# Performance work log

Hardware: AMD Instinct MI355X
Metric: run time of the kernel (lower is better)

## Reference

```python
import jax, jax.numpy as jnp
import numpy as np

D = 128          # embed_features
N = 4096         # cells per batch
M = 8192         # genes / regions
FB1, FB2, FR, FA = 100, 100, 256, 512


def setup_inputs() -> dict:
    key = jax.random.key(0)
    ks = jax.random.split(key, 16)
    s = 0.05  # weight scale to keep activations in a sane range
    return {
        "u1": jax.random.normal(ks[0], (N, FB1), jnp.float32),
        "u2": jax.random.normal(ks[1], (N, FB2), jnp.float32),
        "v1": jax.random.normal(ks[2], (M, FR), jnp.float32),
        "v2": jax.random.normal(ks[3], (M, FA), jnp.float32),
        # linear layers stored as [in, out] so y = x @ W
        "Wb1": jax.random.normal(ks[4], (FB1, D), jnp.float32) * s,
        "Wb2": jax.random.normal(ks[5], (FB2, D), jnp.float32) * s,
        "Wrna1": jax.random.normal(ks[6], (FR, 2 * D), jnp.float32) * s,
        "Wrna2": jax.random.normal(ks[7], (2 * D, D), jnp.float32) * s,
        "gene_act": jax.random.normal(ks[8], (FA, FR), jnp.float32) * s,
        "w_prod1": jax.random.normal(ks[9], (D,), jnp.float32),
        "w_add1": jax.random.normal(ks[10], (2 * D,), jnp.float32),
        "w_prod2": jax.random.normal(ks[11], (D,), jnp.float32),
        "w_add2": jax.random.normal(ks[12], (2 * D,), jnp.float32),
        "bias_1": jax.random.normal(ks[13], (), jnp.float32),
        "bias_2": jax.random.normal(ks[14], (), jnp.float32),
    }


def _pair_scores(eu, ev, w_prod, w_add, bias):
    # Algebraically identical to the original all-pairs form:
    #   (eu[:,None,:] * ev[None,:,:]) @ w_prod  ==  (eu * w_prod) @ ev.T
    #   cat(eu, ev) @ w_add  ==  eu @ w_add[:D]  +  ev @ w_add[D:]
    prod = (eu * w_prod) @ ev.T                     # [N, M]
    add = (eu @ w_add[:D])[:, None] + (ev @ w_add[D:])[None, :]
    return prod + add + bias                        # [N, M]


def reference(u1, u2, v1, v2, Wb1, Wb2, Wrna1, Wrna2, gene_act,
              w_prod1, w_add1, w_prod2, w_add2, bias_1, bias_2):
    # mode='linear' activations -> identity
    embed_u1 = u1 @ Wb1                                          # [N, D]
    embed_v1 = jax.nn.relu(v1 @ Wrna1) @ Wrna2                   # [M, D]
    out1 = jax.nn.relu(_pair_scores(embed_u1, embed_v1, w_prod1, w_add1, bias_1))

    embed_u2 = u2 @ Wb2                                          # [N, D]
    embed_v2 = jax.nn.relu((v2 @ gene_act) @ Wrna1) @ Wrna2      # [M, D]
    out2 = jax.nn.sigmoid(_pair_scores(embed_u2, embed_v2, w_prod2, w_add2, bias_2))

    return out1, out2, embed_u1, embed_v1, embed_u2, embed_v2
```

## Files before the change

### kernel.cpp

```cpp
#include <hip/hip_runtime.h>
#include <math.h>

#define N_CELLS 4096
#define M_GENES 8192

typedef __attribute__((ext_vector_type(8))) short short8;
typedef __attribute__((ext_vector_type(4))) float f32x4;

__device__ __align__(16) float g_a[24576];

__device__ __align__(16) short g_bu1[N_CELLS * 128];
__device__ __align__(16) short g_bv1[M_GENES * 128];
__device__ __align__(16) short g_bu2[N_CELLS * 128];
__device__ __align__(16) short g_bv2[M_GENES * 128];

__device__ __align__(16) short g_gaT[256 * 512];
__device__ __align__(16) short g_W1T[256 * 256];
__device__ __align__(16) short g_W2T[128 * 256];


__device__ __forceinline__ short* bf_sel(int s) {
    switch (s) {
        case 0:  return g_bu1;
        case 1:  return g_bv1;
        case 2:  return g_bu2;
        default: return g_bv2;
    }
}

__device__ __forceinline__ const short* wt_sel(int s) {
    switch (s) {
        case 0:  return g_gaT;
        case 1:  return g_W1T;
        default: return g_W2T;
    }
}

__device__ __forceinline__ short f2bf(float f) {
    unsigned u = __builtin_bit_cast(unsigned, f);
    u += 0x7FFFu + ((u >> 16) & 1u);
    return (short)(u >> 16);
}

__device__ __forceinline__ void cvt8(const float* __restrict__ in, short* __restrict__ out) {
    const float4 x0 = *reinterpret_cast<const float4*>(in);
    const float4 x1 = *reinterpret_cast<const float4*>(in + 4);
    short8 o;
    o[0] = f2bf(x0.x); o[1] = f2bf(x0.y); o[2] = f2bf(x0.z); o[3] = f2bf(x0.w);
    o[4] = f2bf(x1.x); o[5] = f2bf(x1.y); o[6] = f2bf(x1.z); o[7] = f2bf(x1.w);
    *reinterpret_cast<short8*>(out) = o;
}

__device__ __forceinline__ void transpose8(const float* __restrict__ in, short* __restrict__ out,
                                           int c, int K, int Nc) {
    const int o0 = c * 8;
    const int ncol = o0 / K;
    const int k0 = o0 % K;
    short8 o;
#pragma unroll
    for (int j = 0; j < 8; ++j) o[j] = f2bf(in[(size_t)(k0 + j) * Nc + ncol]);
    *reinterpret_cast<short8*>(out + o0) = o;
}

struct Job {
    const short* A;
    const float* Af;
    short* outb_ptr;
    float* outf;
    const float* w_addv;
    int bt_sel;
    int outb_sel;
    int a_ofs;
    int K;
    int relu;
    int nx;
};

__device__ __forceinline__ void chain_block(const Job& j, int b,
                                            short* sAs, short* sBs, float* sRow)
{
    const int t = threadIdx.x, l = t & 63;
    const int bx = (j.nx == 2) ? (b & 1) : 0;
    const int by = (j.nx == 2) ? (b >> 1) : b;
    const int row0 = by * 64, col0 = bx * 128;
    const int K = j.K, Nc = j.nx * 128;
    const short* BT = wt_sel(j.bt_sel);
    short* outb = (j.outb_sel >= 0) ? bf_sel(j.outb_sel) : j.outb_ptr;
    const int w = t >> 6, wm = (w >> 1) * 32, wn = (w & 1) * 64;
    const int lr = l & 15, lkb = (l >> 4) * 16;
    char* cA = (char*)sAs;
    char* cB = (char*)sBs;

    f32x4 acc[2][4] = {};
    for (int k0 = 0; k0 < K; k0 += 128) {
        if (j.Af) {
            const float* gAf = j.Af + (size_t)row0 * K + k0;
#pragma unroll
            for (int c = 0; c < 4; ++c) {
                const int idx = c * 256 + t;
                const int row = idx >> 4, sub = idx & 15;
                const int dst = row * 256 + ((sub * 16) ^ ((row & 7) << 4));
                cvt8(gAf + (size_t)row * K + sub * 8, (short*)(cA + dst));
            }
        } else {
            const char* gA = (const char*)(j.A + (size_t)row0 * K + k0);
#pragma unroll
            for (int c = 0; c < 4; ++c) {
                const int idx = c * 256 + t;
                const int row = idx >> 4, sub = idx & 15;
                const int dst = row * 256 + ((sub * 16) ^ ((row & 7) << 4));
                *(short8*)(cA + dst) = *(const short8*)(gA + (size_t)row * (2 * K) + sub * 16);
            }
        }
        {
            const char* gB = (const char*)(BT + (size_t)col0 * K + k0);
#pragma unroll
            for (int c = 0; c < 8; ++c) {
                const int idx = c * 256 + t;
                const int row = idx >> 4, sub = idx & 15;
                const int dst = row * 256 + ((sub * 16) ^ ((row & 7) << 4));
                *(short8*)(cB + dst) = *(const short8*)(gB + (size_t)row * (2 * K) + sub * 16);
            }
        }
        __syncthreads();
#pragma unroll
        for (int kk = 0; kk < 4; ++kk) {
            const int kb = kk * 64 + lkb;
            short8 a[2], bfr[4];
#pragma unroll
            for (int i = 0; i < 2; ++i) {
                const int rowA = wm + i * 16 + lr;
                a[i] = *(const short8*)(cA + rowA * 256 + (kb ^ ((rowA & 7) << 4)));
            }
#pragma unroll
            for (int jj = 0; jj < 4; ++jj) {
                const int rowB = wn + jj * 16 + lr;
                bfr[jj] = *(const short8*)(cB + rowB * 256 + (kb ^ ((rowB & 7) << 4)));
            }
#pragma unroll
            for (int i = 0; i < 2; ++i)
#pragma unroll
                for (int jj = 0; jj < 4; ++jj)
                    acc[i][jj] = __builtin_amdgcn_mfma_f32_16x16x32_bf16(a[i], bfr[jj], acc[i][jj], 0, 0, 0);
        }
        __syncthreads();
    }

    const int r4 = (l >> 4) * 4;
    const bool rd = (j.w_addv != nullptr);
    float wv[4], part[2][4];
    if (rd) {
#pragma unroll
        for (int jj = 0; jj < 4; ++jj) wv[jj] = j.w_addv[wn + jj * 16 + lr];
#pragma unroll
        for (int i = 0; i < 2; ++i)
#pragma unroll
            for (int r = 0; r < 4; ++r) part[i][r] = 0.f;
    }
#pragma unroll
    for (int i = 0; i < 2; ++i) {
#pragma unroll
        for (int r = 0; r < 4; ++r) {
            const int grow = row0 + wm + i * 16 + r4 + r;
#pragma unroll
            for (int jj = 0; jj < 4; ++jj) {
                float x = acc[i][jj][r];
                if (j.relu) x = fmaxf(x, 0.f);
                const size_t oi = (size_t)grow * Nc + col0 + wn + jj * 16 + lr;
                outb[oi] = f2bf(x);
                if (j.outf) j.outf[oi] = x;
                if (rd) part[i][r] = fmaf(x, wv[jj], part[i][r]);
            }
        }
    }
    if (rd) {
#pragma unroll
        for (int off = 1; off < 16; off <<= 1)
#pragma unroll
            for (int i = 0; i < 2; ++i)
#pragma unroll
                for (int r = 0; r < 4; ++r)
                    part[i][r] += __shfl_xor(part[i][r], off, 64);
        if (t < 64) sRow[t] = 0.f;
        __syncthreads();
        if ((l & 15) == 0) {
#pragma unroll
            for (int i = 0; i < 2; ++i)
#pragma unroll
                for (int r = 0; r < 4; ++r)
                    atomicAdd(&sRow[wm + i * 16 + r4 + r], part[i][r]);
        }
        __syncthreads();
        if (t < 64) g_a[j.a_ofs + row0 + t] = sRow[t];
    }
}

__device__ __forceinline__ void pair_block(int which, int bb, short* sAs, short* sBs,
                                           const float* bias1, const float* bias2,
                                           float* out1, float* out2)
{
    const int t = threadIdx.x, l = t & 63;
    const int col0 = (bb & 63) * 128;
    const int row0 = (bb >> 6) * 128;
    char* cA = (char*)sAs;
    char* cB = (char*)sBs;
    {
        const short8* gA = reinterpret_cast<const short8*>(bf_sel(which ? 2 : 0)) + (size_t)row0 * 16;
        const short8* gB = reinterpret_cast<const short8*>(bf_sel(which ? 3 : 1)) + (size_t)col0 * 16;
#pragma unroll
        for (int c = 0; c < 8; ++c) {
            const int idx = c * 256 + t;
            const int row = idx >> 4, sub = idx & 15;
            const int dst = row * 256 + ((sub * 16) ^ ((row & 7) << 4));
            const short8 va = gA[idx];
            const short8 vb = gB[idx];
            *(short8*)(cA + dst) = va;
            *(short8*)(cB + dst) = vb;
        }
    }
    __syncthreads();

    const int w  = t >> 6;
    const int wm = (w >> 1) * 64;
    const int wn = (w & 1) * 64;
    const int lr = l & 15;
    const int lkb = (l >> 4) * 16;

    f32x4 acc[4][4] = {};
#pragma unroll
    for (int kk = 0; kk < 4; ++kk) {
        const int kb = kk * 64 + lkb;
        short8 a[4], bfr[4];
#pragma unroll
        for (int i = 0; i < 4; ++i) {
            const int rowA = wm + i * 16 + lr;
            a[i] = *(const short8*)(cA + rowA * 256 + (kb ^ ((rowA & 7) << 4)));
            const int rowB = wn + i * 16 + lr;
            bfr[i] = *(const short8*)(cB + rowB * 256 + (kb ^ ((rowB & 7) << 4)));
        }
#pragma unroll
        for (int i = 0; i < 4; ++i)
#pragma unroll
            for (int jj = 0; jj < 4; ++jj)
                acc[i][jj] = __builtin_amdgcn_mfma_f32_16x16x32_bf16(a[i], bfr[jj], acc[i][jj], 0, 0, 0);
    }

    const float bias = which ? *bias2 : *bias1;
    float* outp = which ? out2 : out1;
    const int ofsU = which ? 12288 : 0;
    const int ofsV = which ? 16384 : 4096;
    const int r4 = (l >> 4) * 4;
    float au[4][4];
#pragma unroll
    for (int i = 0; i < 4; ++i)
#pragma unroll
        for (int r = 0; r < 4; ++r)
            au[i][r] = g_a[ofsU + row0 + wm + i * 16 + r4 + r];
    float av[4];
#pragma unroll
    for (int jj = 0; jj < 4; ++jj)
        av[jj] = g_a[ofsV + col0 + wn + jj * 16 + lr];

#pragma unroll
    for (int i = 0; i < 4; ++i) {
#pragma unroll
        for (int r = 0; r < 4; ++r) {
            const int grow = row0 + wm + i * 16 + r4 + r;
            float* orow = outp + (size_t)grow * M_GENES + col0 + wn;
#pragma unroll
            for (int jj = 0; jj < 4; ++jj) {
                float x = acc[i][jj][r] + au[i][r] + av[jj] + bias;
                if (which == 0) x = fmaxf(x, 0.f);
                else            x = __builtin_amdgcn_rcpf(1.f + __expf(-x));
                orow[jj * 16 + lr] = x;
            }
        }
    }
}

__device__ __forceinline__ void embed_block(int b,
        const float* u1, const float* u2, const float* Wb1, const float* Wb2,
        const float* wp1, const float* wa1, const float* wp2, const float* wa2,
        float* eu1, float* eu2, float* sF)
{
    float* sU = sF;
    float* s2 = sF + 256;
    const int t = threadIdx.x;
    const int which = (b >= 2048) ? 1 : 0;
    const int bl = which ? (b - 2048) : b;
    const float* u      = which ? u2 : u1;
    const float* Wb     = which ? Wb2 : Wb1;
    const float* w_prod = which ? wp2 : wp1;
    const float* w_add  = which ? wa2 : wa1;
    float* e            = which ? eu2 : eu1;
    short* bu           = bf_sel(which ? 2 : 0);
    const int a_ofs     = which ? 12288 : 0;
    const int half = t >> 7;
    const int row = bl * 2 + half;
    const int d = t & 127;
    if (d < 100) sU[half * 128 + d] = u[row * 100 + d];
    __syncthreads();
    float acc = 0.f;
#pragma unroll
    for (int k = 0; k < 100; ++k) acc = fmaf(sU[half * 128 + k], Wb[k * 128 + d], acc);
    e[row * 128 + d] = acc;
    bu[row * 128 + d] = f2bf(acc * w_prod[d]);
    float v = acc * w_add[d];
#pragma unroll
    for (int off = 32; off > 0; off >>= 1) v += __shfl_down(v, off, 64);
    if ((t & 63) == 0) s2[t >> 6] = v;
    __syncthreads();
    if (t == 0)   g_a[a_ofs + row] = s2[0] + s2[1];
    if (t == 128) g_a[a_ofs + row] = s2[2] + s2[3];
}

__global__ __launch_bounds__(256) void prep_w(const float* __restrict__ gene_act,
                                              const float* __restrict__ W1,
                                              const float* __restrict__ W2)
{
    const int b = blockIdx.x, t = threadIdx.x;
    if (b < 64)      transpose8(gene_act, g_gaT, b * 256 + t, 512, 256);
    else if (b < 96) transpose8(W1, g_W1T, (b - 64) * 256 + t, 256, 256);
    else             transpose8(W2, g_W2T, (b - 96) * 256 + t, 256, 128);
}

__global__ __launch_bounds__(256) void chain_embed(Job j0, Job j1, int split, int nchain,
        const float* u1, const float* u2, const float* Wb1, const float* Wb2,
        const float* wp1, const float* wa1, const float* wp2, const float* wa2,
        float* eu1, float* eu2)
{
    __shared__ __align__(16) short sMem[24576];
    __shared__ float sF[264];
    const int b = blockIdx.x;
    if (b < nchain) {
        if (b < split) chain_block(j0, b, sMem, sMem + 8192, sF);
        else           chain_block(j1, b - split, sMem, sMem + 8192, sF);
    } else {
        embed_block(b - nchain, u1, u2, Wb1, Wb2, wp1, wa1, wp2, wa2, eu1, eu2, sF);
    }
}

__global__ __launch_bounds__(256) void pair_chain(Job j, int nchain, int which,
        const float* bias1, const float* bias2, float* out1, float* out2)
{
    __shared__ __align__(16) short sMem[32768];
    __shared__ float sF[264];
    const int b = blockIdx.x;
    if (b < nchain) chain_block(j, b, sMem, sMem + 8192, sF);
    else            pair_block(which, b - nchain, sMem, sMem + 16384, bias1, bias2, out1, out2);
}

extern "C" void kernel_launch(void* const* d_in, const int* in_sizes, int n_in,
                              void* d_out, int out_size, void* d_ws, size_t ws_size,
                              hipStream_t stream)
{
    const float* u1       = (const float*)d_in[0];
    const float* u2       = (const float*)d_in[1];
    const float* v1       = (const float*)d_in[2];
    const float* v2       = (const float*)d_in[3];
    const float* Wb1      = (const float*)d_in[4];
    const float* Wb2      = (const float*)d_in[5];
    const float* Wrna1    = (const float*)d_in[6];
    const float* Wrna2    = (const float*)d_in[7];
    const float* gene_act = (const float*)d_in[8];
    const float* w_prod1  = (const float*)d_in[9];
    const float* w_add1   = (const float*)d_in[10];
    const float* w_prod2  = (const float*)d_in[11];
    const float* w_add2   = (const float*)d_in[12];
    const float* bias1    = (const float*)d_in[13];
    const float* bias2    = (const float*)d_in[14];

    float* out  = (float*)d_out;
    float* out1 = out;
    float* out2 = out1 + (size_t)N_CELLS * M_GENES;
    float* eu1  = out2 + (size_t)N_CELLS * M_GENES;
    float* ev1  = eu1 + N_CELLS * 128;
    float* eu2  = ev1 + M_GENES * 128;
    float* ev2  = eu2 + N_CELLS * 128;

    short* H0  = (short*)out2;
    short* H1  = H0 + (size_t)M_GENES * 256;
    short* H0b = H1 + (size_t)M_GENES * 256;

    prep_w<<<112, 256, 0, stream>>>(gene_act, Wrna1, Wrna2);

    Job jH1 = { nullptr, v2, H1, nullptr, nullptr, 0, -1, 0,     512, 0, 2 };
    Job jH0 = { nullptr, v1, H0, nullptr, nullptr, 1, -1, 0,     256, 1, 2 };
    chain_embed<<<4608, 256, 0, stream>>>(jH1, jH0, 256, 512,
        u1, u2, Wb1, Wb2, w_prod1, w_add1, w_prod2, w_add2, eu1, eu2);

    Job jev1 = { H0, nullptr, nullptr, ev1, w_add1 + 128, 2, 1, 4096,  256, 0, 1 };
    Job jH0b = { H1, nullptr, H0b, nullptr, nullptr,      1, -1, 0,    256, 1, 2 };
    chain_embed<<<384, 256, 0, stream>>>(jev1, jH0b, 128, 384,
        u1, u2, Wb1, Wb2, w_prod1, w_add1, w_prod2, w_add2, eu1, eu2);

    Job jev2 = { H0b, nullptr, nullptr, ev2, w_add2 + 128, 2, 3, 16384, 256, 0, 1 };
    pair_chain<<<2176, 256, 0, stream>>>(jev2, 128, 0, bias1, bias2, out1, out2);

    Job jnull = {};
    pair_chain<<<2048, 256, 0, stream>>>(jnull, 0, 1, bias1, bias2, out1, out2);
}
```

Before: 112.1 us.

## Fuse MLP chain layers per row tile in LDS and merge pair kernels

Each 64-row tile of v1/v2 now runs the whole embedding MLP in one block, keeping intermediate hidden activations in shared memory. This replaces the multi-launch chain that wrote bf16 hidden buffers to global memory. The cell embedding is reworked to handle 8 rows per block with the weights staged in LDS, and the two pair-score launches are merged into one 3D grid. The cost is a long serial chain of small-tile MFMA stages and syncs within only 256 heavy blocks, which may underfill the GPU compared with the previous wider launches.

Measured after the change: 114.7 us. 1.02x slower.

```diff
diff --git a/kernel.cpp b/kernel.cpp
--- a/kernel.cpp
+++ b/kernel.cpp
@@ -62,151 +62,320 @@
     *reinterpret_cast<short8*>(out + o0) = o;
 }
 
-struct Job {
-    const short* A;
-    const float* Af;
-    short* outb_ptr;
-    float* outf;
-    const float* w_addv;
-    int bt_sel;
-    int outb_sel;
-    int a_ofs;
-    int K;
-    int relu;
-    int nx;
-};
-
-__device__ __forceinline__ void chain_block(const Job& j, int b,
-                                            short* sAs, short* sBs, float* sRow)
-{
-    const int t = threadIdx.x, l = t & 63;
-    const int bx = (j.nx == 2) ? (b & 1) : 0;
-    const int by = (j.nx == 2) ? (b >> 1) : b;
-    const int row0 = by * 64, col0 = bx * 128;
-    const int K = j.K, Nc = j.nx * 128;
-    const short* BT = wt_sel(j.bt_sel);
-    short* outb = (j.outb_sel >= 0) ? bf_sel(j.outb_sel) : j.outb_ptr;
-    const int w = t >> 6, wm = (w >> 1) * 32, wn = (w & 1) * 64;
+__device__ __forceinline__ void stage_A_f32(char* cA, const float* Af, int row0, int k0, int K, int t)
+{
+    const float* gAf = Af + (size_t)row0 * K + k0;
+#pragma unroll
+    for (int c = 0; c < 4; ++c) {
+        const int idx = c * 256 + t;
+        const int row = idx >> 4, sub = idx & 15;
+        const int dst = row * 256 + ((sub * 16) ^ ((row & 7) << 4));
+        cvt8(gAf + (size_t)row * K + sub * 8, (short*)(cA + dst));
+    }
+}
+
+__device__ __forceinline__ void stage_B128(char* cB, const short* BT, int col0, int k0, int K, int t)
+{
+    const char* gB = (const char*)(BT + (size_t)col0 * K + k0);
+#pragma unroll
+    for (int c = 0; c < 8; ++c) {
+        const int idx = c * 256 + t;
+        const int row = idx >> 4, sub = idx & 15;
+        const int dst = row * 256 + ((sub * 16) ^ ((row & 7) << 4));
+        *(short8*)(cB + dst) = *(const short8*)(gB + (size_t)row * (2 * K) + sub * 16);
+    }
+}
+
+__device__ __forceinline__ void stage_B64(char* cB, const short* BT, int col0, int k0, int K, int t)
+{
+    const char* gB = (const char*)(BT + (size_t)col0 * K + k0);
+#pragma unroll
+    for (int c = 0; c < 4; ++c) {
+        const int idx = c * 256 + t;
+        const int row = idx >> 4, sub = idx & 15;
+        const int dst = row * 256 + ((sub * 16) ^ ((row & 7) << 4));
+        *(short8*)(cB + dst) = *(const short8*)(gB + (size_t)row * (2 * K) + sub * 16);
+    }
+}
+
+__device__ __forceinline__ void mfma128(const char* cA, int strideA, int baseA,
+                                        const char* cB, f32x4 (&acc)[2][4], int t)
+{
+    const int l = t & 63, w = t >> 6;
+    const int wm = (w >> 1) * 32, wn = (w & 1) * 64;
     const int lr = l & 15, lkb = (l >> 4) * 16;
-    char* cA = (char*)sAs;
-    char* cB = (char*)sBs;
-
-    f32x4 acc[2][4] = {};
-    for (int k0 = 0; k0 < K; k0 += 128) {
-        if (j.Af) {
-            const float* gAf = j.Af + (size_t)row0 * K + k0;
-#pragma unroll
-            for (int c = 0; c < 4; ++c) {
-                const int idx = c * 256 + t;
-                const int row = idx >> 4, sub = idx & 15;
-                const int dst = row * 256 + ((sub * 16) ^ ((row & 7) << 4));
-                cvt8(gAf + (size_t)row * K + sub * 8, (short*)(cA + dst));
-            }
-        } else {
-            const char* gA = (const char*)(j.A + (size_t)row0 * K + k0);
-#pragma unroll
-            for (int c = 0; c < 4; ++c) {
-                const int idx = c * 256 + t;
-                const int row = idx >> 4, sub = idx & 15;
-                const int dst = row * 256 + ((sub * 16) ^ ((row & 7) << 4));
-                *(short8*)(cA + dst) = *(const short8*)(gA + (size_t)row * (2 * K) + sub * 16);
-            }
-        }
-        {
-            const char* gB = (const char*)(BT + (size_t)col0 * K + k0);
-#pragma unroll
-            for (int c = 0; c < 8; ++c) {
-                const int idx = c * 256 + t;
-                const int row = idx >> 4, sub = idx & 15;
-                const int dst = row * 256 + ((sub * 16) ^ ((row & 7) << 4));
-                *(short8*)(cB + dst) = *(const short8*)(gB + (size_t)row * (2 * K) + sub * 16);
-            }
-        }
-        __syncthreads();
-#pragma unroll
-        for (int kk = 0; kk < 4; ++kk) {
-            const int kb = kk * 64 + lkb;
-            short8 a[2], bfr[4];
-#pragma unroll
-            for (int i = 0; i < 2; ++i) {
-                const int rowA = wm + i * 16 + lr;
-                a[i] = *(const short8*)(cA + rowA * 256 + (kb ^ ((rowA & 7) << 4)));
-            }
-#pragma unroll
-            for (int jj = 0; jj < 4; ++jj) {
-                const int rowB = wn + jj * 16 + lr;
-                bfr[jj] = *(const short8*)(cB + rowB * 256 + (kb ^ ((rowB & 7) << 4)));
-            }
-#pragma unroll
-            for (int i = 0; i < 2; ++i)
-#pragma unroll
-                for (int jj = 0; jj < 4; ++jj)
-                    acc[i][jj] = __builtin_amdgcn_mfma_f32_16x16x32_bf16(a[i], bfr[jj], acc[i][jj], 0, 0, 0);
-        }
-        __syncthreads();
-    }
-
-    const int r4 = (l >> 4) * 4;
-    const bool rd = (j.w_addv != nullptr);
-    float wv[4], part[2][4];
-    if (rd) {
-#pragma unroll
-        for (int jj = 0; jj < 4; ++jj) wv[jj] = j.w_addv[wn + jj * 16 + lr];
+#pragma unroll
+    for (int kk = 0; kk < 4; ++kk) {
+        const int kb = kk * 64 + lkb;
+        short8 a[2], b4[4];
+#pragma unroll
+        for (int i = 0; i < 2; ++i) {
+            const int rA = wm + i * 16 + lr;
+            a[i] = *(const short8*)(cA + rA * strideA + ((baseA + kb) ^ ((rA & 7) << 4)));
+        }
+#pragma unroll
+        for (int jj = 0; jj < 4; ++jj) {
+            const int rB = wn + jj * 16 + lr;
+            b4[jj] = *(const short8*)(cB + rB * 256 + (kb ^ ((rB & 7) << 4)));
+        }
 #pragma unroll
         for (int i = 0; i < 2; ++i)
 #pragma unroll
-            for (int r = 0; r < 4; ++r) part[i][r] = 0.f;
-    }
-#pragma unroll
-    for (int i = 0; i < 2; ++i) {
+            for (int jj = 0; jj < 4; ++jj)
+                acc[i][jj] = __builtin_amdgcn_mfma_f32_16x16x32_bf16(a[i], b4[jj], acc[i][jj], 0, 0, 0);
+    }
+}
+
+__device__ __forceinline__ void mfma64(const char* cA, int strideA, int baseA,
+                                       const char* cB, f32x4 (&acc)[4], int t)
+{
+    const int l = t & 63, w = t >> 6;
+    const int wm = w * 16;
+    const int lr = l & 15, lkb = (l >> 4) * 16;
+#pragma unroll
+    for (int kk = 0; kk < 4; ++kk) {
+        const int kb = kk * 64 + lkb;
+        const int rA = wm + lr;
+        const short8 a = *(const short8*)(cA + rA * strideA + ((baseA + kb) ^ ((rA & 7) << 4)));
+#pragma unroll
+        for (int jj = 0; jj < 4; ++jj) {
+            const int rB = jj * 16 + lr;
+            const short8 b = *(const short8*)(cB + rB * 256 + (kb ^ ((rB & 7) << 4)));
+            acc[jj] = __builtin_amdgcn_mfma_f32_16x16x32_bf16(a, b, acc[jj], 0, 0, 0);
+        }
+    }
+}
+
+__device__ __forceinline__ void acc_to_sH(char* sH, const f32x4 (&acc)[2][4], int ct, bool relu, int t)
+{
+    const int l = t & 63, w = t >> 6;
+    const int wm = (w >> 1) * 32, wn = (w & 1) * 64;
+    const int lr = l & 15, r4 = (l >> 4) * 4;
+#pragma unroll
+    for (int i = 0; i < 2; ++i)
 #pragma unroll
         for (int r = 0; r < 4; ++r) {
-            const int grow = row0 + wm + i * 16 + r4 + r;
+            const int row = wm + i * 16 + r4 + r;
 #pragma unroll
             for (int jj = 0; jj < 4; ++jj) {
                 float x = acc[i][jj][r];
-                if (j.relu) x = fmaxf(x, 0.f);
-                const size_t oi = (size_t)grow * Nc + col0 + wn + jj * 16 + lr;
-                outb[oi] = f2bf(x);
-                if (j.outf) j.outf[oi] = x;
-                if (rd) part[i][r] = fmaf(x, wv[jj], part[i][r]);
+                if (relu) x = fmaxf(x, 0.f);
+                const int col = ct * 128 + wn + jj * 16 + lr;
+                *(short*)(sH + row * 512 + ((col * 2) ^ ((row & 7) << 4))) = f2bf(x);
             }
         }
-    }
-    if (rd) {
-#pragma unroll
-        for (int off = 1; off < 16; off <<= 1)
-#pragma unroll
-            for (int i = 0; i < 2; ++i)
-#pragma unroll
-                for (int r = 0; r < 4; ++r)
-                    part[i][r] += __shfl_xor(part[i][r], off, 64);
-        if (t < 64) sRow[t] = 0.f;
+}
+
+__device__ __forceinline__ void acc2_to_sH(char* sH, const f32x4 (&a4)[4], int ct, bool relu, int t)
+{
+    const int l = t & 63, w = t >> 6;
+    const int lr = l & 15, r4 = (l >> 4) * 4;
+#pragma unroll
+    for (int r = 0; r < 4; ++r) {
+        const int row = w * 16 + r4 + r;
+#pragma unroll
+        for (int jj = 0; jj < 4; ++jj) {
+            float x = a4[jj][r];
+            if (relu) x = fmaxf(x, 0.f);
+            const int col = ct * 64 + jj * 16 + lr;
+            *(short*)(sH + row * 512 + ((col * 2) ^ ((row & 7) << 4))) = f2bf(x);
+        }
+    }
+}
+
+__device__ __forceinline__ void first_layer(const float* Vf, int row0, int KV, int bsel, bool relu,
+                                            char* cA, char* cH, int t)
+{
+    const short* BT = wt_sel(bsel);
+    f32x4 accA[2][4] = {}, accB[2][4] = {};
+    for (int k0 = 0; k0 < KV; k0 += 128) {
+        stage_A_f32(cA, Vf, row0, k0, KV, t);
+        stage_B128(cH, BT, 0, k0, KV, t);
         __syncthreads();
-        if ((l & 15) == 0) {
-#pragma unroll
-            for (int i = 0; i < 2; ++i)
-#pragma unroll
-                for (int r = 0; r < 4; ++r)
-                    atomicAdd(&sRow[wm + i * 16 + r4 + r], part[i][r]);
-        }
+        mfma128(cA, 256, 0, cH, accA, t);
         __syncthreads();
-        if (t < 64) g_a[j.a_ofs + row0 + t] = sRow[t];
-    }
-}
-
-__device__ __forceinline__ void pair_block(int which, int bb, short* sAs, short* sBs,
-                                           const float* bias1, const float* bias2,
-                                           float* out1, float* out2)
-{
-    const int t = threadIdx.x, l = t & 63;
-    const int col0 = (bb & 63) * 128;
-    const int row0 = (bb >> 6) * 128;
-    char* cA = (char*)sAs;
-    char* cB = (char*)sBs;
+        stage_B128(cH, BT, 128, k0, KV, t);
+        __syncthreads();
+        mfma128(cA, 256, 0, cH, accB, t);
+        __syncthreads();
+    }
+    acc_to_sH(cH, accA, 0, relu, t);
+    acc_to_sH(cH, accB, 1, relu, t);
+    __syncthreads();
+}
+
+__device__ __forceinline__ void mid_layer(char* cH, char* cB64, int t)
+{
+    const short* W1T = wt_sel(1);
+    f32x4 h4[4][4];
+#pragma unroll
+    for (int ct = 0; ct < 4; ++ct)
+#pragma unroll
+        for (int jj = 0; jj < 4; ++jj) h4[ct][jj] = (f32x4){0.f, 0.f, 0.f, 0.f};
+#pragma unroll
+    for (int ct = 0; ct < 4; ++ct)
+        for (int k0 = 0; k0 < 2; ++k0) {
+            stage_B64(cB64, W1T, ct * 64, k0 * 128, 256, t);
+            __syncthreads();
+            mfma64(cH, 512, k0 * 256, cB64, h4[ct], t);
+            __syncthreads();
+        }
+#pragma unroll
+    for (int ct = 0; ct < 4; ++ct) acc2_to_sH(cH, h4[ct], ct, true, t);
+    __syncthreads();
+}
+
+__device__ __forceinline__ void final_layer(char* cH, char* cB64, float* evout, short* bv,
+                                            const float* w_add_hi, int a_ofs, int row0, int t)
+{
+    const short* W2T = wt_sel(2);
+    const int l = t & 63, w = t >> 6, lr = l & 15, r4 = (l >> 4) * 4;
+    float part[4] = {0.f, 0.f, 0.f, 0.f};
+#pragma unroll
+    for (int ct = 0; ct < 2; ++ct) {
+        f32x4 a2[4] = {};
+        for (int k0 = 0; k0 < 2; ++k0) {
+            stage_B64(cB64, W2T, ct * 64, k0 * 128, 256, t);
+            __syncthreads();
+            mfma64(cH, 512, k0 * 256, cB64, a2, t);
+            __syncthreads();
+        }
+#pragma unroll
+        for (int r = 0; r < 4; ++r) {
+            const int grow = row0 + w * 16 + r4 + r;
+#pragma unroll
+            for (int jj = 0; jj < 4; ++jj) {
+                const float x = a2[jj][r];
+                const int col = ct * 64 + jj * 16 + lr;
+                evout[(size_t)grow * 128 + col] = x;
+                bv[(size_t)grow * 128 + col] = f2bf(x);
+                part[r] = fmaf(x, w_add_hi[col], part[r]);
+            }
+        }
+    }
+#pragma unroll
+    for (int off = 1; off < 16; off <<= 1)
+#pragma unroll
+        for (int r = 0; r < 4; ++r) part[r] += __shfl_xor(part[r], off, 64);
+    if (lr == 0) {
+#pragma unroll
+        for (int r = 0; r < 4; ++r) g_a[a_ofs + row0 + w * 16 + r4 + r] = part[r];
+    }
+}
+
+__device__ __forceinline__ void embed8(int be, const float* u1, const float* u2,
+        const float* Wb1, const float* Wb2, const float* wp1, const float* wa1,
+        const float* wp2, const float* wa2, float* eu1, float* eu2, float* sMemF)
+{
+    const int which = (be >= 512) ? 1 : 0;
+    const int bl = which ? (be - 512) : be;
+    const float* u  = which ? u2 : u1;
+    const float* Wb = which ? Wb2 : Wb1;
+    const float* wp = which ? wp2 : wp1;
+    const float* wa = which ? wa2 : wa1;
+    float* e  = which ? eu2 : eu1;
+    short* bu = bf_sel(which ? 2 : 0);
+    const int a_ofs = which ? 12288 : 0;
+    const int row0 = bl * 8;
+    float* sWb = sMemF;
+    float* sUu = sMemF + 12800;
+    float* sF  = sMemF + 13600;
+    const int t = threadIdx.x;
+    for (int c = t; c < 3200; c += 256)
+        ((float4*)sWb)[c] = ((const float4*)Wb)[c];
+    for (int c = t; c < 800; c += 256) sUu[c] = u[row0 * 100 + c];
+    if (t < 8) sF[t] = 0.f;
+    __syncthreads();
+    const int d = t & 127, g = t >> 7;
+    float acc[4] = {0.f, 0.f, 0.f, 0.f};
+    for (int k = 0; k < 100; ++k) {
+        const float wv = sWb[k * 128 + d];
+#pragma unroll
+        for (int rr = 0; rr < 4; ++rr) acc[rr] = fmaf(wv, sUu[(g * 4 + rr) * 100 + k], acc[rr]);
+    }
+    const float wpd = wp[d], wad = wa[d];
+    float pv[4];
+#pragma unroll
+    for (int rr = 0; rr < 4; ++rr) {
+        const int row = row0 + g * 4 + rr;
+        e[(size_t)row * 128 + d] = acc[rr];
+        bu[(size_t)row * 128 + d] = f2bf(acc[rr] * wpd);
+        pv[rr] = acc[rr] * wad;
+    }
+#pragma unroll
+    for (int off = 32; off > 0; off >>= 1)
+#pragma unroll
+        for (int rr = 0; rr < 4; ++rr) pv[rr] += __shfl_down(pv[rr], off, 64);
+    if ((t & 63) == 0) {
+#pragma unroll
+        for (int rr = 0; rr < 4; ++rr) atomicAdd(&sF[g * 4 + rr], pv[rr]);
+    }
+    __syncthreads();
+    if (t < 8) g_a[a_ofs + row0 + t] = sF[t];
+}
+
+__global__ __launch_bounds__(256) void prep_w(const float* __restrict__ gene_act,
+                                              const float* __restrict__ W1,
+                                              const float* __restrict__ W2)
+{
+    const int b = blockIdx.x, t = threadIdx.x;
+    if (b < 64)      transpose8(gene_act, g_gaT, b * 256 + t, 512, 256);
+    else if (b < 96) transpose8(W1, g_W1T, (b - 64) * 256 + t, 256, 256);
+    else             transpose8(W2, g_W2T, (b - 96) * 256 + t, 256, 128);
+}
+
+__global__ __launch_bounds__(256) void fused_mid(const float* __restrict__ v1,
+                                                 const float* __restrict__ v2,
+                                                 const float* __restrict__ u1,
+                                                 const float* __restrict__ u2,
+                                                 const float* __restrict__ Wb1,
+                                                 const float* __restrict__ Wb2,
+                                                 const float* __restrict__ wp1,
+                                                 const float* __restrict__ wa1,
+                                                 const float* __restrict__ wp2,
+                                                 const float* __restrict__ wa2,
+                                                 float* __restrict__ eu1,
+                                                 float* __restrict__ eu2,
+                                                 float* __restrict__ ev1,
+                                                 float* __restrict__ ev2)
+{
+    __shared__ __align__(16) short sMem[32768];
+    char* cA   = (char*)sMem;
+    char* cB64 = cA + 16384;
+    char* cH   = cA + 32768;
+    const int b = blockIdx.x, t = threadIdx.x;
+    if (b < 128) {
+        const int row0 = b * 64;
+        first_layer(v2, row0, 512, 0, false, cA, cH, t);
+        mid_layer(cH, cB64, t);
+        final_layer(cH, cB64, ev2, bf_sel(3), wa2 + 128, 16384, row0, t);
+    } else if (b < 256) {
+        const int row0 = (b - 128) * 64;
+        first_layer(v1, row0, 256, 1, true, cA, cH, t);
+        final_layer(cH, cB64, ev1, bf_sel(1), wa1 + 128, 4096, row0, t);
+    } else {
+        embed8(b - 256, u1, u2, Wb1, Wb2, wp1, wa1, wp2, wa2, eu1, eu2, (float*)sMem);
+    }
+}
+
+__global__ __launch_bounds__(256) void pair_both(const float* __restrict__ bias1,
+                                                 const float* __restrict__ bias2,
+                                                 float* __restrict__ out1,
+                                                 float* __restrict__ out2)
+{
+    __shared__ __align__(16) short sA[128 * 128];
+    __shared__ __align__(16) short sB[128 * 128];
+    const int which = blockIdx.z;
+    const int t = threadIdx.x;
+    const int l = t & 63;
+    const int row0 = blockIdx.y * 128;
+    const int col0 = blockIdx.x * 128;
+
     {
         const short8* gA = reinterpret_cast<const short8*>(bf_sel(which ? 2 : 0)) + (size_t)row0 * 16;
         const short8* gB = reinterpret_cast<const short8*>(bf_sel(which ? 3 : 1)) + (size_t)col0 * 16;
+        char* cA = (char*)sA;
+        char* cB = (char*)sB;
 #pragma unroll
         for (int c = 0; c < 8; ++c) {
             const int idx = c * 256 + t;
@@ -227,6 +396,8 @@
     const int lkb = (l >> 4) * 16;
 
     f32x4 acc[4][4] = {};
+    const char* cA = (const char*)sA;
+    const char* cB = (const char*)sB;
 #pragma unroll
     for (int kk = 0; kk < 4; ++kk) {
         const int kb = kk * 64 + lkb;
@@ -276,78 +447,6 @@
             }
         }
     }
-}
-
-__device__ __forceinline__ void embed_block(int b,
-        const float* u1, const float* u2, const float* Wb1, const float* Wb2,
-        const float* wp1, const float* wa1, const float* wp2, const float* wa2,
-        float* eu1, float* eu2, float* sF)
-{
-    float* sU = sF;
-    float* s2 = sF + 256;
-    const int t = threadIdx.x;
-    const int which = (b >= 2048) ? 1 : 0;
-    const int bl = which ? (b - 2048) : b;
-    const float* u      = which ? u2 : u1;
-    const float* Wb     = which ? Wb2 : Wb1;
-    const float* w_prod = which ? wp2 : wp1;
-    const float* w_add  = which ? wa2 : wa1;
-    float* e            = which ? eu2 : eu1;
-    short* bu           = bf_sel(which ? 2 : 0);
-    const int a_ofs     = which ? 12288 : 0;
-    const int half = t >> 7;
-    const int row = bl * 2 + half;
-    const int d = t & 127;
-    if (d < 100) sU[half * 128 + d] = u[row * 100 + d];
-    __syncthreads();
-    float acc = 0.f;
-#pragma unroll
-    for (int k = 0; k < 100; ++k) acc = fmaf(sU[half * 128 + k], Wb[k * 128 + d], acc);
-    e[row * 128 + d] = acc;
-    bu[row * 128 + d] = f2bf(acc * w_prod[d]);
-    float v = acc * w_add[d];
-#pragma unroll
-    for (int off = 32; off > 0; off >>= 1) v += __shfl_down(v, off, 64);
-    if ((t & 63) == 0) s2[t >> 6] = v;
-    __syncthreads();
-    if (t == 0)   g_a[a_ofs + row] = s2[0] + s2[1];
-    if (t == 128) g_a[a_ofs + row] = s2[2] + s2[3];
-}
-
-__global__ __launch_bounds__(256) void prep_w(const float* __restrict__ gene_act,
-                                              const float* __restrict__ W1,
-                                              const float* __restrict__ W2)
-{
-    const int b = blockIdx.x, t = threadIdx.x;
-    if (b < 64)      transpose8(gene_act, g_gaT, b * 256 + t, 512, 256);
-    else if (b < 96) transpose8(W1, g_W1T, (b - 64) * 256 + t, 256, 256);
-    else             transpose8(W2, g_W2T, (b - 96) * 256 + t, 256, 128);
-}
-
-__global__ __launch_bounds__(256) void chain_embed(Job j0, Job j1, int split, int nchain,
-        const float* u1, const float* u2, const float* Wb1, const float* Wb2,
-        const float* wp1, const float* wa1, const float* wp2, const float* wa2,
-        float* eu1, float* eu2)
-{
-    __shared__ __align__(16) short sMem[24576];
-    __shared__ float sF[264];
-    const int b = blockIdx.x;
-    if (b < nchain) {
-        if (b < split) chain_block(j0, b, sMem, sMem + 8192, sF);
-        else           chain_block(j1, b - split, sMem, sMem + 8192, sF);
-    } else {
-        embed_block(b - nchain, u1, u2, Wb1, Wb2, wp1, wa1, wp2, wa2, eu1, eu2, sF);
-    }
-}
-
-__global__ __launch_bounds__(256) void pair_chain(Job j, int nchain, int which,
-        const float* bias1, const float* bias2, float* out1, float* out2)
-{
-    __shared__ __align__(16) short sMem[32768];
-    __shared__ float sF[264];
-    const int b = blockIdx.x;
-    if (b < nchain) chain_block(j, b, sMem, sMem + 8192, sF);
-    else            pair_block(which, b - nchain, sMem, sMem + 16384, bias1, bias2, out1, out2);
 }
 
 extern "C" void kernel_launch(void* const* d_in, const int* in_sizes, int n_in,
@@ -378,25 +477,11 @@
     float* eu2  = ev1 + M_GENES * 128;
     float* ev2  = eu2 + N_CELLS * 128;
 
-    short* H0  = (short*)out2;
-    short* H1  = H0 + (size_t)M_GENES * 256;
-    short* H0b = H1 + (size_t)M_GENES * 256;
-
     prep_w<<<112, 256, 0, stream>>>(gene_act, Wrna1, Wrna2);
 
-    Job jH1 = { nullptr, v2, H1, nullptr, nullptr, 0, -1, 0,     512, 0, 2 };
-    Job jH0 = { nullptr, v1, H0, nullptr, nullptr, 1, -1, 0,     256, 1, 2 };
-    chain_embed<<<4608, 256, 0, stream>>>(jH1, jH0, 256, 512,
-        u1, u2, Wb1, Wb2, w_prod1, w_add1, w_prod2, w_add2, eu1, eu2);
-
-    Job jev1 = { H0, nullptr, nullptr, ev1, w_add1 + 128, 2, 1, 4096,  256, 0, 1 };
-    Job jH0b = { H1, nullptr, H0b, nullptr, nullptr,      1, -1, 0,    256, 1, 2 };
-    chain_embed<<<384, 256, 0, stream>>>(jev1, jH0b, 128, 384,
-        u1, u2, Wb1, Wb2, w_prod1, w_add1, w_prod2, w_add2, eu1, eu2);
-
-    Job jev2 = { H0b, nullptr, nullptr, ev2, w_add2 + 128, 2, 3, 16384, 256, 0, 1 };
-    pair_chain<<<2176, 256, 0, stream>>>(jev2, 128, 0, bias1, bias2, out1, out2);
-
-    Job jnull = {};
-    pair_chain<<<2048, 256, 0, stream>>>(jnull, 0, 1, bias1, bias2, out1, out2);
-}
+    fused_mid<<<1280, 256, 0, stream>>>(v1, v2, u1, u2, Wb1, Wb2,
+                                        w_prod1, w_add1, w_prod2, w_add2,
+                                        eu1, eu2, ev1, ev2);
+
+    pair_both<<<dim3(64, 32, 2), 256, 0, stream>>>(bias1, bias2, out1, out2);
+}
```
